# Kernel tuning notes

Hardware: AMD Instinct MI355X
Metric: run time of the kernel (lower is better)

## Reference

```python
import jax, jax.numpy as jnp
import numpy as np

NUM_HEADS = 8
KEY_DIM = 256
EPS = 1e-16


def setup_inputs() -> dict:
    key = jax.random.key(0)
    k1, k2, k3, k4 = jax.random.split(key, 4)
    b, n, d, m = 2, 20000, 256, 320000
    q = jax.random.normal(k1, (b, n, d), dtype=jnp.float32)
    k = jax.random.normal(k2, (b, n, d), dtype=jnp.float32)
    e = jax.random.randint(k3, (2, m), 0, n, dtype=jnp.int64)
    r = jax.random.randint(k4, (m,), 0, n, dtype=jnp.int64)
    return {"q": q, "k": k, "e": e, "r": r}


def reference(q, k, e, r):
    b, n, d = q.shape
    m = e.shape[1]
    dh = d // NUM_HEADS
    # gather edge endpoints, multiply, sum within each head's d_head chunk
    # (scatter_sum over dim with h=[i//dh] == reshape + sum over last axis)
    src_q = q[:, e[0], :]                      # (b, m, d)
    dst_k = k[:, e[1], :]                      # (b, m, d)
    a = (src_q * dst_k).reshape(b, m, NUM_HEADS, dh).sum(-1)  # (b, m, H)
    a = a / jnp.sqrt(jnp.asarray(KEY_DIM, a.dtype))
    # segment softmax over edges grouped by r (global max subtraction, as in source)
    a = a - a.max()
    ex = jnp.exp(a)                            # (b, m, H)
    seg = jax.ops.segment_sum(ex.transpose(1, 0, 2), r, num_segments=n)  # (n, b, H)
    denom = seg[r].transpose(1, 0, 2)          # (b, m, H)
    return ex / (denom + EPS)
```

## Files before the change

### kernel.cpp

```cpp
#include <hip/hip_runtime.h>
#include <hip/hip_bf16.h>
#include <cmath>

#define D 256
#define NH 8
#define B 2
#define EPW 8
#define EPW32 4

__device__ inline unsigned short f2bf(float f) {
    unsigned u = __float_as_uint(f);
    unsigned r = u + 0x7FFFu + ((u >> 16) & 1u);
    return (unsigned short)(r >> 16);
}

__global__ __launch_bounds__(256) void k_conv(
    const float* __restrict__ q, const float* __restrict__ k,
    uint4* __restrict__ qc, uint4* __restrict__ kc, int n)
{
    int total = n * B * 32;
    for (int i = blockIdx.x * blockDim.x + threadIdx.x; i < total;
         i += gridDim.x * blockDim.x) {
        int c   = i & 31;
        int row = i >> 5;
        int bb  = (row >= n) ? 1 : 0;
        int node = row - bb * n;
        const float4* qs = (const float4*)(q + ((size_t)row << 8)) + (c << 1);
        const float4* ks = (const float4*)(k + ((size_t)row << 8)) + (c << 1);
        float4 a0 = qs[0], a1 = qs[1];
        float4 b0 = ks[0], b1 = ks[1];
        uint4 pa, pb;
        pa.x = (unsigned)f2bf(a0.x) | ((unsigned)f2bf(a0.y) << 16);
        pa.y = (unsigned)f2bf(a0.z) | ((unsigned)f2bf(a0.w) << 16);
        pa.z = (unsigned)f2bf(a1.x) | ((unsigned)f2bf(a1.y) << 16);
        pa.w = (unsigned)f2bf(a1.z) | ((unsigned)f2bf(a1.w) << 16);
        pb.x = (unsigned)f2bf(b0.x) | ((unsigned)f2bf(b0.y) << 16);
        pb.y = (unsigned)f2bf(b0.z) | ((unsigned)f2bf(b0.w) << 16);
        pb.z = (unsigned)f2bf(b1.x) | ((unsigned)f2bf(b1.y) << 16);
        pb.w = (unsigned)f2bf(b1.z) | ((unsigned)f2bf(b1.w) << 16);
        size_t dst = ((size_t)node * B + bb) * 32 + c;
        qc[dst] = pa;
        kc[dst] = pb;
    }
}

__global__ __launch_bounds__(256) void k_scores_fused(
    const ushort* __restrict__ qc, const ushort* __restrict__ kc,
    const int* __restrict__ e, const int* __restrict__ r,
    float* __restrict__ s, float* __restrict__ seg, int m)
{
    int wave = (int)((blockIdx.x * blockDim.x + threadIdx.x) >> 6);
    int lane = threadIdx.x & 63;
    int j0 = wave * EPW;
    if (j0 >= m) return;

    int rr[EPW];
    uint4 qa[EPW], kb[EPW];
    #pragma unroll
    for (int t = 0; t < EPW; ++t) {
        int j = j0 + t;
        int ok = (j < m);
        int e0 = ok ? e[j]     : 0;
        int e1 = ok ? e[m + j] : 0;
        rr[t] = ok ? r[j]      : 0;
        qa[t] = ((const uint4*)(qc + (size_t)e0 * (B * D)))[lane];
        kb[t] = ((const uint4*)(kc + (size_t)e1 * (B * D)))[lane];
    }
    __builtin_amdgcn_sched_barrier(0);

    #pragma unroll
    for (int t = 0; t < EPW; ++t) {
        float p = 0.f;
        const unsigned* qw = (const unsigned*)&qa[t];
        const unsigned* kw = (const unsigned*)&kb[t];
        #pragma unroll
        for (int w = 0; w < 4; ++w) {
            float ql = __uint_as_float(qw[w] << 16);
            float qh = __uint_as_float(qw[w] & 0xFFFF0000u);
            float kl = __uint_as_float(kw[w] << 16);
            float kh = __uint_as_float(kw[w] & 0xFFFF0000u);
            p = fmaf(ql, kl, p);
            p = fmaf(qh, kh, p);
        }
        p += __shfl_xor(p, 1);
        p += __shfl_xor(p, 2);
        float ex = __expf(p * 0.0625f);
        if ((lane & 3) == 0 && (j0 + t) < m) {
            int bb = lane >> 5;
            int h  = (lane >> 2) & 7;
            s[((size_t)bb * m + (j0 + t)) * NH + h] = ex;
            atomicAdd(&seg[((size_t)rr[t] * B + bb) * NH + h], ex);
        }
    }
}

__global__ __launch_bounds__(256) void k_scores_fused_f32(
    const float* __restrict__ q, const float* __restrict__ k,
    const int* __restrict__ e, const int* __restrict__ r,
    float* __restrict__ s, float* __restrict__ seg, int n, int m)
{
    int wave = (int)((blockIdx.x * blockDim.x + threadIdx.x) >> 6);
    int lane = threadIdx.x & 63;
    int j0 = wave * EPW32;
    if (j0 >= m) return;
    int e0[EPW32], e1[EPW32], rr[EPW32];
    #pragma unroll
    for (int t = 0; t < EPW32; ++t) {
        int j = j0 + t; int ok = (j < m);
        e0[t] = ok ? e[j] : 0; e1[t] = ok ? e[m + j] : 0; rr[t] = ok ? r[j] : 0;
    }
    float4 qa[B][EPW32], kb[B][EPW32];
    #pragma unroll
    for (int bb = 0; bb < B; ++bb)
        #pragma unroll
        for (int t = 0; t < EPW32; ++t) {
            qa[bb][t] = ((const float4*)(q + ((size_t)bb * n + e0[t]) * D))[lane];
            kb[bb][t] = ((const float4*)(k + ((size_t)bb * n + e1[t]) * D))[lane];
        }
    __builtin_amdgcn_sched_barrier(0);
    #pragma unroll
    for (int bb = 0; bb < B; ++bb)
        #pragma unroll
        for (int t = 0; t < EPW32; ++t) {
            float4 A = qa[bb][t], K4 = kb[bb][t];
            float p = A.x * K4.x + A.y * K4.y + A.z * K4.z + A.w * K4.w;
            p += __shfl_xor(p, 1); p += __shfl_xor(p, 2); p += __shfl_xor(p, 4);
            float ex = __expf(p * 0.0625f);
            if ((lane & 7) == 0 && (j0 + t) < m) {
                int h = lane >> 3;
                s[((size_t)bb * m + (j0 + t)) * NH + h] = ex;
                atomicAdd(&seg[((size_t)rr[t] * B + bb) * NH + h], ex);
            }
        }
}

__global__ __launch_bounds__(256) void k_norm(
    float* __restrict__ s, const int* __restrict__ r,
    const float* __restrict__ seg, int m)
{
    int i = blockIdx.x * blockDim.x + threadIdx.x;
    int total = B * m;
    if (i >= total) return;
    int bb = (i >= m) ? 1 : 0;
    int j  = i - bb * m;
    const float4* sg = (const float4*)(seg + ((size_t)r[j] * B + bb) * NH);
    float4* sp = (float4*)(s + (size_t)i * NH);
    float4 d0 = sg[0], d1 = sg[1];
    float4 x0 = sp[0], x1 = sp[1];
    x0.x = __fdividef(x0.x, d0.x + 1e-16f);
    x0.y = __fdividef(x0.y, d0.y + 1e-16f);
    x0.z = __fdividef(x0.z, d0.z + 1e-16f);
    x0.w = __fdividef(x0.w, d0.w + 1e-16f);
    x1.x = __fdividef(x1.x, d1.x + 1e-16f);
    x1.y = __fdividef(x1.y, d1.y + 1e-16f);
    x1.z = __fdividef(x1.z, d1.z + 1e-16f);
    x1.w = __fdividef(x1.w, d1.w + 1e-16f);
    sp[0] = x0; sp[1] = x1;
}

extern "C" void kernel_launch(void* const* d_in, const int* in_sizes, int n_in,
                              void* d_out, int out_size, void* d_ws, size_t ws_size,
                              hipStream_t stream) {
    const float* q = (const float*)d_in[0];
    const float* k = (const float*)d_in[1];
    const int*   e = (const int*)d_in[2];
    const int*   r = (const int*)d_in[3];
    float* s = (float*)d_out;

    int n = in_sizes[0] / (B * D);
    int m = in_sizes[3];

    size_t seg_bytes = (size_t)n * B * NH * sizeof(float);
    size_t row_bytes = (size_t)n * B * D * sizeof(unsigned short);
    float*  seg = (float*)d_ws;
    ushort* qc  = (ushort*)((char*)d_ws + seg_bytes);
    ushort* kc  = (ushort*)((char*)d_ws + seg_bytes + row_bytes);
    bool use_bf16 = ws_size >= (seg_bytes + 2 * row_bytes);

    hipMemsetAsync(d_ws, 0, seg_bytes, stream);

    int nblocks = (B * m + 255) / 256;

    if (use_bf16) {
        int cblocks = (n * B * 32 + 255) / 256;
        int nwaves  = (m + EPW - 1) / EPW;
        int sblocks = (nwaves + 3) / 4;
        k_conv<<<cblocks, 256, 0, stream>>>(q, k, (uint4*)qc, (uint4*)kc, n);
        k_scores_fused<<<sblocks, 256, 0, stream>>>(qc, kc, e, r, s, seg, m);
    } else {
        int nwaves  = (m + EPW32 - 1) / EPW32;
        int sblocks = (nwaves + 3) / 4;
        k_scores_fused_f32<<<sblocks, 256, 0, stream>>>(q, k, e, r, s, seg, n, m);
    }
    k_norm<<<nblocks, 256, 0, stream>>>(s, r, seg, m);
}
```

Baseline: 226.5 us.

## Bucket-sort edges by source node to improve gather locality in score kernel

Adds a histogram, scan and scatter pass that groups edges into buckets of 64 source nodes, writing a permutation of (src, dst, r, original index). The score kernel then walks edges in this order so that q-row gathers hit cache more often, and it swizzles block order across the XCDs. Edges per wave drop from 8 to 4. The cost is three extra launches, a global-atomic scatter and a 16-byte-per-edge permutation buffer. The scattered output writes also lose their original ordering.

```diff
diff --git a/kernel.cpp b/kernel.cpp
--- a/kernel.cpp
+++ b/kernel.cpp
@@ -5,8 +5,8 @@
 #define D 256
 #define NH 8
 #define B 2
-#define EPW 8
-#define EPW32 4
+#define EPW 4
+#define NBMAX 512
 
 __device__ inline unsigned short f2bf(float f) {
     unsigned u = __float_as_uint(f);
@@ -44,29 +44,75 @@
     }
 }
 
-__global__ __launch_bounds__(256) void k_scores_fused(
+__global__ __launch_bounds__(256) void k_hist(
+    const int* __restrict__ e, int* __restrict__ hist, int m)
+{
+    __shared__ int lh[NBMAX];
+    for (int t = threadIdx.x; t < NBMAX; t += 256) lh[t] = 0;
+    __syncthreads();
+    for (int j = blockIdx.x * blockDim.x + threadIdx.x; j < m;
+         j += gridDim.x * blockDim.x)
+        atomicAdd(&lh[e[j] >> 6], 1);
+    __syncthreads();
+    for (int t = threadIdx.x; t < NBMAX; t += 256)
+        if (lh[t]) atomicAdd(&hist[t], lh[t]);
+}
+
+__global__ __launch_bounds__(NBMAX) void k_scan(
+    const int* __restrict__ hist, int* __restrict__ cursor)
+{
+    __shared__ int tmp[NBMAX];
+    int t = threadIdx.x;
+    int own = hist[t];
+    tmp[t] = own;
+    __syncthreads();
+    for (int off = 1; off < NBMAX; off <<= 1) {
+        int v = (t >= off) ? tmp[t - off] : 0;
+        __syncthreads();
+        tmp[t] += v;
+        __syncthreads();
+    }
+    cursor[t] = tmp[t] - own;
+}
+
+__global__ __launch_bounds__(256) void k_scatter(
+    const int* __restrict__ e, const int* __restrict__ r,
+    int* __restrict__ cursor, int4* __restrict__ perm, int m)
+{
+    for (int j = blockIdx.x * blockDim.x + threadIdx.x; j < m;
+         j += gridDim.x * blockDim.x) {
+        int e0 = e[j];
+        int pos = atomicAdd(&cursor[e0 >> 6], 1);
+        perm[pos] = make_int4(e0, e[m + j], r[j], j);
+    }
+}
+
+__global__ __launch_bounds__(256) void k_scores_perm(
     const ushort* __restrict__ qc, const ushort* __restrict__ kc,
-    const int* __restrict__ e, const int* __restrict__ r,
-    float* __restrict__ s, float* __restrict__ seg, int m)
-{
-    int wave = (int)((blockIdx.x * blockDim.x + threadIdx.x) >> 6);
+    const int4* __restrict__ perm,
+    float* __restrict__ s, float* __restrict__ seg, int m, int do_swz)
+{
+    int bid = blockIdx.x;
+    if (do_swz) {
+        int nb8 = gridDim.x >> 3;
+        bid = (bid & 7) * nb8 + (bid >> 3);
+    }
+    int wave = (bid << 2) + (threadIdx.x >> 6);
     int lane = threadIdx.x & 63;
     int j0 = wave * EPW;
     if (j0 >= m) return;
 
-    int rr[EPW];
+    int rr[EPW], jo[EPW];
     uint4 qa[EPW], kb[EPW];
     #pragma unroll
     for (int t = 0; t < EPW; ++t) {
         int j = j0 + t;
-        int ok = (j < m);
-        int e0 = ok ? e[j]     : 0;
-        int e1 = ok ? e[m + j] : 0;
-        rr[t] = ok ? r[j]      : 0;
-        qa[t] = ((const uint4*)(qc + (size_t)e0 * (B * D)))[lane];
-        kb[t] = ((const uint4*)(kc + (size_t)e1 * (B * D)))[lane];
-    }
-    __builtin_amdgcn_sched_barrier(0);
+        int4 p = (j < m) ? perm[j] : make_int4(0, 0, 0, -1);
+        rr[t] = p.z;
+        jo[t] = p.w;
+        qa[t] = ((const uint4*)(qc + (size_t)p.x * (B * D)))[lane];
+        kb[t] = ((const uint4*)(kc + (size_t)p.y * (B * D)))[lane];
+    }
 
     #pragma unroll
     for (int t = 0; t < EPW; ++t) {
@@ -85,6 +131,57 @@
         p += __shfl_xor(p, 1);
         p += __shfl_xor(p, 2);
         float ex = __expf(p * 0.0625f);
+        if ((lane & 3) == 0 && jo[t] >= 0) {
+            int bb = lane >> 5;
+            int h  = (lane >> 2) & 7;
+            s[((size_t)bb * m + jo[t]) * NH + h] = ex;
+            atomicAdd(&seg[((size_t)rr[t] * B + bb) * NH + h], ex);
+        }
+    }
+}
+
+__global__ __launch_bounds__(256) void k_scores_fused(
+    const ushort* __restrict__ qc, const ushort* __restrict__ kc,
+    const int* __restrict__ e, const int* __restrict__ r,
+    float* __restrict__ s, float* __restrict__ seg, int m)
+{
+    int wave = (int)((blockIdx.x * blockDim.x + threadIdx.x) >> 6);
+    int lane = threadIdx.x & 63;
+    int j0 = wave * EPW;
+    if (j0 >= m) return;
+
+    int e0[EPW], e1[EPW], rr[EPW];
+    #pragma unroll
+    for (int t = 0; t < EPW; ++t) {
+        int j = j0 + t;
+        int ok = (j < m);
+        e0[t] = ok ? e[j]     : 0;
+        e1[t] = ok ? e[m + j] : 0;
+        rr[t] = ok ? r[j]     : 0;
+    }
+    uint4 qa[EPW], kb[EPW];
+    #pragma unroll
+    for (int t = 0; t < EPW; ++t) {
+        qa[t] = ((const uint4*)(qc + (size_t)e0[t] * (B * D)))[lane];
+        kb[t] = ((const uint4*)(kc + (size_t)e1[t] * (B * D)))[lane];
+    }
+    #pragma unroll
+    for (int t = 0; t < EPW; ++t) {
+        float p = 0.f;
+        const unsigned* qw = (const unsigned*)&qa[t];
+        const unsigned* kw = (const unsigned*)&kb[t];
+        #pragma unroll
+        for (int w = 0; w < 4; ++w) {
+            float ql = __uint_as_float(qw[w] << 16);
+            float qh = __uint_as_float(qw[w] & 0xFFFF0000u);
+            float kl = __uint_as_float(kw[w] << 16);
+            float kh = __uint_as_float(kw[w] & 0xFFFF0000u);
+            p = fmaf(ql, kl, p);
+            p = fmaf(qh, kh, p);
+        }
+        p += __shfl_xor(p, 1);
+        p += __shfl_xor(p, 2);
+        float ex = __expf(p * 0.0625f);
         if ((lane & 3) == 0 && (j0 + t) < m) {
             int bb = lane >> 5;
             int h  = (lane >> 2) & 7;
@@ -101,27 +198,26 @@
 {
     int wave = (int)((blockIdx.x * blockDim.x + threadIdx.x) >> 6);
     int lane = threadIdx.x & 63;
-    int j0 = wave * EPW32;
+    int j0 = wave * EPW;
     if (j0 >= m) return;
-    int e0[EPW32], e1[EPW32], rr[EPW32];
-    #pragma unroll
-    for (int t = 0; t < EPW32; ++t) {
+    int e0[EPW], e1[EPW], rr[EPW];
+    #pragma unroll
+    for (int t = 0; t < EPW; ++t) {
         int j = j0 + t; int ok = (j < m);
         e0[t] = ok ? e[j] : 0; e1[t] = ok ? e[m + j] : 0; rr[t] = ok ? r[j] : 0;
     }
-    float4 qa[B][EPW32], kb[B][EPW32];
+    float4 qa[B][EPW], kb[B][EPW];
     #pragma unroll
     for (int bb = 0; bb < B; ++bb)
         #pragma unroll
-        for (int t = 0; t < EPW32; ++t) {
+        for (int t = 0; t < EPW; ++t) {
             qa[bb][t] = ((const float4*)(q + ((size_t)bb * n + e0[t]) * D))[lane];
             kb[bb][t] = ((const float4*)(k + ((size_t)bb * n + e1[t]) * D))[lane];
         }
-    __builtin_amdgcn_sched_barrier(0);
     #pragma unroll
     for (int bb = 0; bb < B; ++bb)
         #pragma unroll
-        for (int t = 0; t < EPW32; ++t) {
+        for (int t = 0; t < EPW; ++t) {
             float4 A = qa[bb][t], K4 = kb[bb][t];
             float p = A.x * K4.x + A.y * K4.y + A.z * K4.z + A.w * K4.w;
             p += __shfl_xor(p, 1); p += __shfl_xor(p, 2); p += __shfl_xor(p, 4);
@@ -170,26 +266,42 @@
     int n = in_sizes[0] / (B * D);
     int m = in_sizes[3];
 
-    size_t seg_bytes = (size_t)n * B * NH * sizeof(float);
-    size_t row_bytes = (size_t)n * B * D * sizeof(unsigned short);
-    float*  seg = (float*)d_ws;
-    ushort* qc  = (ushort*)((char*)d_ws + seg_bytes);
-    ushort* kc  = (ushort*)((char*)d_ws + seg_bytes + row_bytes);
-    bool use_bf16 = ws_size >= (seg_bytes + 2 * row_bytes);
-
-    hipMemsetAsync(d_ws, 0, seg_bytes, stream);
+    size_t seg_bytes  = (size_t)n * B * NH * sizeof(float);
+    size_t sort_meta  = 2 * NBMAX * sizeof(int);
+    size_t row_bytes  = (size_t)n * B * D * sizeof(unsigned short);
+    size_t perm_bytes = (size_t)m * sizeof(int4);
+
+    float* seg    = (float*)d_ws;
+    int*   hist   = (int*)((char*)d_ws + seg_bytes);
+    int*   cursor = hist + NBMAX;
+    ushort* qc = (ushort*)((char*)d_ws + seg_bytes + sort_meta);
+    ushort* kc = (ushort*)((char*)d_ws + seg_bytes + sort_meta + row_bytes);
+    int4*  perm = (int4*)((char*)d_ws + seg_bytes + sort_meta + 2 * row_bytes);
+
+    bool use_bf16 = ws_size >= (seg_bytes + sort_meta + 2 * row_bytes);
+    bool use_sort = use_bf16 &&
+                    ws_size >= (seg_bytes + sort_meta + 2 * row_bytes + perm_bytes) &&
+                    ((n + 63) >> 6) <= NBMAX;
+
+    hipMemsetAsync(d_ws, 0, seg_bytes + sort_meta, stream);
 
     int nblocks = (B * m + 255) / 256;
+    int nwaves  = (m + EPW - 1) / EPW;
+    int sblocks = (nwaves + 3) / 4;
 
     if (use_bf16) {
         int cblocks = (n * B * 32 + 255) / 256;
-        int nwaves  = (m + EPW - 1) / EPW;
-        int sblocks = (nwaves + 3) / 4;
         k_conv<<<cblocks, 256, 0, stream>>>(q, k, (uint4*)qc, (uint4*)kc, n);
-        k_scores_fused<<<sblocks, 256, 0, stream>>>(qc, kc, e, r, s, seg, m);
+        if (use_sort) {
+            k_hist<<<256, 256, 0, stream>>>(e, hist, m);
+            k_scan<<<1, NBMAX, 0, stream>>>(hist, cursor);
+            k_scatter<<<256, 256, 0, stream>>>(e, r, cursor, perm, m);
+            int do_swz = (sblocks % 8 == 0) ? 1 : 0;
+            k_scores_perm<<<sblocks, 256, 0, stream>>>(qc, kc, perm, s, seg, m, do_swz);
+        } else {
+            k_scores_fused<<<sblocks, 256, 0, stream>>>(qc, kc, e, r, s, seg, m);
+        }
     } else {
-        int nwaves  = (m + EPW32 - 1) / EPW32;
-        int sblocks = (nwaves + 3) / 4;
         k_scores_fused_f32<<<sblocks, 256, 0, stream>>>(q, k, e, r, s, seg, n, m);
     }
     k_norm<<<nblocks, 256, 0, stream>>>(s, r, seg, m);
```

After: 327.1 us. 1.44x slower.
